# Performance work log

Hardware: AMD Instinct MI355X
Metric: run time of the kernel (lower is better)

## Reference

```python
import jax, jax.numpy as jnp
import numpy as np

N_NODES = 100000
NUM_LAYER = 3
REG_WEIGHT = 1e-4


def setup_inputs() -> dict:
    key = jax.random.key(0)
    ks = jax.random.split(key, 6)
    E = 1280000
    B = 4096
    D = 64
    # xavier-uniform-like scale for embedding table
    emb_weight = jax.random.normal(ks[0], (N_NODES, D), dtype=jnp.float32) * 0.01
    src = jax.random.randint(ks[1], (E,), 0, N_NODES, dtype=jnp.int32)
    dst = jax.random.randint(ks[2], (E,), 0, N_NODES, dtype=jnp.int32)
    users = jax.random.randint(ks[3], (B,), 0, N_NODES, dtype=jnp.int32)
    pos = jax.random.randint(ks[4], (B,), 0, N_NODES, dtype=jnp.int32)
    neg = jax.random.randint(ks[5], (B,), 0, N_NODES, dtype=jnp.int32)
    return {"emb_weight": emb_weight, "src": src, "dst": dst,
            "users": users, "pos": pos, "neg": neg}


def _edge_norm(src, dst):
    # DGL norm(): d = sum of edge mask (ones) per dst node; adj_e = d[src]^-0.5 * d[dst]^-0.5
    ones = jnp.ones(src.shape[0], dtype=jnp.float32)
    deg = jax.ops.segment_sum(ones, dst, num_segments=N_NODES)
    dinv = jnp.where(deg > 0, deg ** -0.5, 0.0)  # inf -> 0 handling
    return dinv[src] * dinv[dst]  # [E]


def _propagate(emb_weight, src, dst, adj):
    # LightGCN propagation: h_{l+1}[v] = sum_{(u->v)} adj_e * h_l[u]
    h = emb_weight
    layers = [h]
    for _ in range(NUM_LAYER):
        m = h[src] * adj[:, None]                    # [E, D] gather + edge weight
        h = jax.ops.segment_sum(m, dst, num_segments=N_NODES)  # [N, D] scatter-sum
        layers.append(h)
    return jnp.mean(jnp.stack(layers, axis=1), axis=1)  # mean over L+1 layers


def reference(emb_weight, src, dst, users, pos, neg):
    adj = _edge_norm(src, dst)
    all_emb = _propagate(emb_weight, src, dst, adj)

    u_e, p_e, n_e = all_emb[users], all_emb[pos], all_emb[neg]
    u0, p0, n0 = emb_weight[users], emb_weight[pos], emb_weight[neg]

    B = users.shape[0]
    reg_loss = 0.5 * (jnp.sum(u0 ** 2) + jnp.sum(p0 ** 2) + jnp.sum(n0 ** 2)) / B
    reg_loss = reg_loss * REG_WEIGHT

    pos_scores = jnp.sum(u_e * p_e, axis=1)
    neg_scores = jnp.sum(u_e * n_e, axis=1)
    loss_emb = jnp.mean(jax.nn.softplus(neg_scores - pos_scores))

    loss = loss_emb + reg_loss
    return loss, loss_emb, reg_loss
```

## Files before the change

### kernel.cpp

```cpp
#include <hip/hip_runtime.h>
#include <hip/hip_fp8.h>
#include <math.h>

#define N_NODES 100000
#define DIM 64
#define NUM_LAYER 3
#define BATCH 4096
#define REG_WEIGHT 1e-4f
#define NBUCKET 391
#define STAGE_CAP 4096
#define CURPAD 16
#define H_SCALE 64.0f
#define H_INV_SCALE (1.0f / 64.0f)

typedef float floatx2 __attribute__((ext_vector_type(2)));

__device__ unsigned char g_hf8[2][(size_t)N_NODES * DIM];
__device__ float g_sums[(size_t)3 * BATCH * DIM];
__device__ int   g_row_ptr[N_NODES + 1];
__device__ float g_dinv[N_NODES];
__device__ int   g_bcur[NBUCKET * CURPAD];
__device__ unsigned int g_stage[NBUCKET * STAGE_CAP];
__device__ int   g_csr[1280000];
__device__ int   g_shead[N_NODES];
__device__ int   g_snext[3 * BATCH];
__device__ float g_part_sp[BATCH];
__device__ float g_part_rg[BATCH];

__device__ inline void fma4_fp8(unsigned int d, float w,
                                float& a0, float& a1, float& a2, float& a3) {
    floatx2 lo = __builtin_amdgcn_cvt_pk_f32_fp8((int)d, false);
    floatx2 hi = __builtin_amdgcn_cvt_pk_f32_fp8((int)d, true);
    a0 = fmaf(w, lo.x, a0); a1 = fmaf(w, lo.y, a1);
    a2 = fmaf(w, hi.x, a2); a3 = fmaf(w, hi.y, a3);
}
__device__ inline unsigned int pack4_fp8(float a0, float a1, float a2, float a3) {
    int w = __builtin_amdgcn_cvt_pk_fp8_f32(a0, a1, 0, false);
    w     = __builtin_amdgcn_cvt_pk_fp8_f32(a2, a3, w, true);
    return (unsigned int)w;
}

__global__ void prelude(const float* __restrict__ emb) {
    int i = blockIdx.x * blockDim.x + threadIdx.x;
    int stride = gridDim.x * blockDim.x;
    for (int k = i; k < NBUCKET; k += stride) g_bcur[k * CURPAD] = k * STAGE_CAP;
    for (int k = i; k < N_NODES; k += stride) g_shead[k] = -1;
    const int NW = N_NODES * DIM / 4;
    unsigned int* hw = (unsigned int*)g_hf8[0];
    for (int k = i; k < NW; k += stride) {
        const float* e = emb + (size_t)k * 4;
        hw[k] = pack4_fp8(e[0] * H_SCALE, e[1] * H_SCALE,
                          e[2] * H_SCALE, e[3] * H_SCALE);
    }
}

#define EDGES_PER_THREAD 8
__global__ void __launch_bounds__(1024) stage_buckets(const int* __restrict__ src,
                                                      const int* __restrict__ dst, int E,
                                                      const int* __restrict__ users,
                                                      const int* __restrict__ pos,
                                                      const int* __restrict__ neg) {
    __shared__ int h[NBUCKET];
    __shared__ int cur[NBUCKET];
    int tid = threadIdx.x;
    int gt = blockIdx.x * 1024 + tid;
    if (gt < 3 * BATCH) {
        int which = gt / BATCH, s = gt - which * BATCH;
        const int* idx = (which == 0) ? users : ((which == 1) ? pos : neg);
        g_snext[gt] = atomicExch(&g_shead[idx[s]], gt);
    }
    int base = blockIdx.x * (1024 * EDGES_PER_THREAD);
    for (int i = tid; i < NBUCKET; i += 1024) h[i] = 0;
    __syncthreads();
    int myd[EDGES_PER_THREAD], mys[EDGES_PER_THREAD];
    #pragma unroll
    for (int k = 0; k < EDGES_PER_THREAD; ++k) {
        int e = base + k * 1024 + tid;
        if (e < E) {
            myd[k] = dst[e]; mys[k] = src[e];
            atomicAdd(&h[myd[k] >> 8], 1);
        } else myd[k] = -1;
    }
    __syncthreads();
    for (int i = tid; i < NBUCKET; i += 1024) {
        int c = h[i];
        cur[i] = c ? atomicAdd(&g_bcur[i * CURPAD], c) : 0;
    }
    __syncthreads();
    #pragma unroll
    for (int k = 0; k < EDGES_PER_THREAD; ++k) {
        if (myd[k] >= 0) {
            int p = atomicAdd(&cur[myd[k] >> 8], 1);
            g_stage[p] = (unsigned int)((mys[k] << 8) | (myd[k] & 255));
        }
    }
}

__global__ void __launch_bounds__(512) finalize_place() {
    __shared__ int cs[512];
    __shared__ int lh[256], sc[256], cur[256];
    int b = blockIdx.x, t = threadIdx.x;
    int c = (t < NBUCKET) ? (g_bcur[t * CURPAD] - t * STAGE_CAP) : 0;
    cs[t] = c;
    __syncthreads();
    for (int off = 1; off < 512; off <<= 1) {
        int x = (t >= off) ? cs[t - off] : 0;
        __syncthreads();
        cs[t] += x;
        __syncthreads();
    }
    int mybase = (b > 0) ? cs[b - 1] : 0;
    int cnt    = cs[b] - mybase;
    if (b == 0 && t == 0) g_row_ptr[N_NODES] = cs[NBUCKET - 1];
    int sbeg = b * STAGE_CAP;
    if (t < 256) lh[t] = 0;
    __syncthreads();
    for (int k = t; k < cnt; k += 512)
        atomicAdd(&lh[g_stage[sbeg + k] & 255], 1);
    __syncthreads();
    int v = 0;
    if (t < 256) { v = lh[t]; sc[t] = v; }
    __syncthreads();
    for (int off = 1; off < 256; off <<= 1) {
        int x = (t >= off && t < 256) ? sc[t - off] : 0;
        __syncthreads();
        if (t < 256) sc[t] += x;
        __syncthreads();
    }
    if (t < 256) {
        int start = mybase + sc[t] - v;
        cur[t] = start;
        int node = (b << 8) + t;
        if (node < N_NODES) {
            g_row_ptr[node] = start;
            g_dinv[node]    = (v > 0) ? rsqrtf((float)v) : 0.0f;
        }
    }
    __syncthreads();
    for (int k = t; k < cnt; k += 512) {
        unsigned int e = g_stage[sbeg + k];
        int pos = atomicAdd(&cur[e & 255], 1);
        g_csr[pos] = (int)(e >> 8);
    }
}

__global__ void pull_layer_fp8(const unsigned char* __restrict__ h,
                               unsigned char* __restrict__ hn, int do_gather) {
    int wid  = (blockIdx.x * blockDim.x + threadIdx.x) >> 6;
    int lane = threadIdx.x & 63;
    int nA = wid * 2, nB = nA + 1;
    if (nA >= N_NODES) return;
    bool hasB = (nB < N_NODES);
    int g  = lane >> 4;
    int li = lane & 15;
    int begA = g_row_ptr[nA], endA = g_row_ptr[nA + 1];
    int begB = hasB ? g_row_ptr[nB] : 0, endB = hasB ? g_row_ptr[nB + 1] : 0;
    float dinvA = g_dinv[nA];
    float dinvB = hasB ? g_dinv[nB] : 0.0f;
    int lenA = endA - begA, lenB = endB - begB;
    int maxLen = max(lenA, lenB);
    float aA0 = 0.f, aA1 = 0.f, aA2 = 0.f, aA3 = 0.f;
    float aB0 = 0.f, aB1 = 0.f, aB2 = 0.f, aB3 = 0.f;
    for (int off = 0; off < maxLen; off += 64) {
        int kA = off + lane;
        int sA = 0; float wA = 0.0f;
        if (kA < lenA) { sA = g_csr[begA + kA]; wA = g_dinv[sA] * dinvA; }
        int sB = 0; float wB = 0.0f;
        if (kA < lenB) { sB = g_csr[begB + kA]; wB = g_dinv[sB] * dinvB; }
        int cnt = min(64, maxLen - off);
        for (int j = 0; j < cnt; j += 16) {
            int   sA1 = __shfl(sA, j + g),      sA2 = __shfl(sA, j + 4 + g);
            int   sA3 = __shfl(sA, j + 8 + g),  sA4 = __shfl(sA, j + 12 + g);
            int   sB1 = __shfl(sB, j + g),      sB2 = __shfl(sB, j + 4 + g);
            int   sB3 = __shfl(sB, j + 8 + g),  sB4 = __shfl(sB, j + 12 + g);
            float wA1 = __shfl(wA, j + g),      wA2 = __shfl(wA, j + 4 + g);
            float wA3 = __shfl(wA, j + 8 + g),  wA4 = __shfl(wA, j + 12 + g);
            float wB1 = __shfl(wB, j + g),      wB2 = __shfl(wB, j + 4 + g);
            float wB3 = __shfl(wB, j + 8 + g),  wB4 = __shfl(wB, j + 12 + g);
            unsigned int dA1 = *(const unsigned int*)(h + (size_t)sA1 * DIM + li * 4);
            unsigned int dA2 = *(const unsigned int*)(h + (size_t)sA2 * DIM + li * 4);
            unsigned int dA3 = *(const unsigned int*)(h + (size_t)sA3 * DIM + li * 4);
            unsigned int dA4 = *(const unsigned int*)(h + (size_t)sA4 * DIM + li * 4);
            unsigned int dB1 = *(const unsigned int*)(h + (size_t)sB1 * DIM + li * 4);
            unsigned int dB2 = *(const unsigned int*)(h + (size_t)sB2 * DIM + li * 4);
            unsigned int dB3 = *(const unsigned int*)(h + (size_t)sB3 * DIM + li * 4);
            unsigned int dB4 = *(const unsigned int*)(h + (size_t)sB4 * DIM + li * 4);
            fma4_fp8(dA1, wA1, aA0, aA1, aA2, aA3);
            fma4_fp8(dA2, wA2, aA0, aA1, aA2, aA3);
            fma4_fp8(dA3, wA3, aA0, aA1, aA2, aA3);
            fma4_fp8(dA4, wA4, aA0, aA1, aA2, aA3);
            fma4_fp8(dB1, wB1, aB0, aB1, aB2, aB3);
            fma4_fp8(dB2, wB2, aB0, aB1, aB2, aB3);
            fma4_fp8(dB3, wB3, aB0, aB1, aB2, aB3);
            fma4_fp8(dB4, wB4, aB0, aB1, aB2, aB3);
        }
    }
    #pragma unroll
    for (int off = 16; off < 64; off <<= 1) {
        aA0 += __shfl_xor(aA0, off); aA1 += __shfl_xor(aA1, off);
        aA2 += __shfl_xor(aA2, off); aA3 += __shfl_xor(aA3, off);
        aB0 += __shfl_xor(aB0, off); aB1 += __shfl_xor(aB1, off);
        aB2 += __shfl_xor(aB2, off); aB3 += __shfl_xor(aB3, off);
    }
    if (lane < 16) {
        *(unsigned int*)(hn + (size_t)nA * DIM + li * 4) = pack4_fp8(aA0, aA1, aA2, aA3);
        if (hasB)
            *(unsigned int*)(hn + (size_t)nB * DIM + li * 4) = pack4_fp8(aB0, aB1, aB2, aB3);
    }
    if (do_gather) {
        int sidx = g_shead[nA];
        while (sidx >= 0) {
            if (lane < 16) {
                float* sp = &g_sums[(size_t)sidx * DIM + li * 4];
                sp[0] = aA0 * H_INV_SCALE; sp[1] = aA1 * H_INV_SCALE;
                sp[2] = aA2 * H_INV_SCALE; sp[3] = aA3 * H_INV_SCALE;
            }
            sidx = g_snext[sidx];
        }
        if (hasB) {
            sidx = g_shead[nB];
            while (sidx >= 0) {
                if (lane < 16) {
                    float* sp = &g_sums[(size_t)sidx * DIM + li * 4];
                    sp[0] = aB0 * H_INV_SCALE; sp[1] = aB1 * H_INV_SCALE;
                    sp[2] = aB2 * H_INV_SCALE; sp[3] = aB3 * H_INV_SCALE;
                }
                sidx = g_snext[sidx];
            }
        }
    }
}

__global__ void pull_sampled(const unsigned char* __restrict__ h,
                             const int* __restrict__ users, const int* __restrict__ pos,
                             const int* __restrict__ neg) {
    int wid  = (blockIdx.x * blockDim.x + threadIdx.x) >> 6;
    int lane = threadIdx.x & 63;
    if (wid >= 3 * BATCH) return;
    int which = wid / BATCH;
    int i     = wid - which * BATCH;
    const int* idx = (which == 0) ? users : ((which == 1) ? pos : neg);
    int node = idx[i];
    int g  = lane >> 4;
    int li = lane & 15;
    int beg = g_row_ptr[node], end = g_row_ptr[node + 1];
    float dinv_d = g_dinv[node];
    float a0 = 0.f, a1 = 0.f, a2 = 0.f, a3 = 0.f;
    for (int base = beg; base < end; base += 64) {
        int k = base + lane;
        int s = 0; float w = 0.0f;
        if (k < end) { s = g_csr[k]; w = g_dinv[s] * dinv_d; }
        int cnt = min(64, end - base);
        for (int j = 0; j < cnt; j += 16) {
            int   sA = __shfl(s, j + g),      sB = __shfl(s, j + 4 + g);
            int   sC = __shfl(s, j + 8 + g),  sD = __shfl(s, j + 12 + g);
            float wA = __shfl(w, j + g),      wB = __shfl(w, j + 4 + g);
            float wC = __shfl(w, j + 8 + g),  wD = __shfl(w, j + 12 + g);
            unsigned int dA = *(const unsigned int*)(h + (size_t)sA * DIM + li * 4);
            unsigned int dB = *(const unsigned int*)(h + (size_t)sB * DIM + li * 4);
            unsigned int dC = *(const unsigned int*)(h + (size_t)sC * DIM + li * 4);
            unsigned int dD = *(const unsigned int*)(h + (size_t)sD * DIM + li * 4);
            fma4_fp8(dA, wA, a0, a1, a2, a3);
            fma4_fp8(dB, wB, a0, a1, a2, a3);
            fma4_fp8(dC, wC, a0, a1, a2, a3);
            fma4_fp8(dD, wD, a0, a1, a2, a3);
        }
    }
    #pragma unroll
    for (int off = 16; off < 64; off <<= 1) {
        a0 += __shfl_xor(a0, off);
        a1 += __shfl_xor(a1, off);
        a2 += __shfl_xor(a2, off);
        a3 += __shfl_xor(a3, off);
    }
    if (lane < 16) {
        unsigned int dn = *(const unsigned int*)(h + (size_t)node * DIM + li * 4);
        floatx2 lo = __builtin_amdgcn_cvt_pk_f32_fp8((int)dn, false);
        floatx2 hi = __builtin_amdgcn_cvt_pk_f32_fp8((int)dn, true);
        float* sp = &g_sums[(size_t)wid * DIM + li * 4];
        sp[0] += (a0 + lo.x) * H_INV_SCALE;
        sp[1] += (a1 + lo.y) * H_INV_SCALE;
        sp[2] += (a2 + hi.x) * H_INV_SCALE;
        sp[3] += (a3 + hi.y) * H_INV_SCALE;
    }
}

__global__ void score_reduce(const float* __restrict__ emb,
                             const int* __restrict__ users, const int* __restrict__ pos,
                             const int* __restrict__ neg) {
    int wid  = (blockIdx.x * blockDim.x + threadIdx.x) >> 6;
    int lane = threadIdx.x & 63;
    if (wid >= BATCH) return;
    float u0 = emb[(size_t)users[wid] * DIM + lane];
    float p0 = emb[(size_t)pos[wid]   * DIM + lane];
    float n0 = emb[(size_t)neg[wid]   * DIM + lane];
    float u = 0.25f * (g_sums[(size_t)wid * DIM + lane] + u0);
    float p = 0.25f * (g_sums[(size_t)(BATCH + wid) * DIM + lane] + p0);
    float n = 0.25f * (g_sums[(size_t)(2 * BATCH + wid) * DIM + lane] + n0);
    float ps = u * p;
    float ns = u * n;
    float rg = u0 * u0 + p0 * p0 + n0 * n0;
    #pragma unroll
    for (int off = 32; off > 0; off >>= 1) {
        ps += __shfl_down(ps, off);
        ns += __shfl_down(ns, off);
        rg += __shfl_down(rg, off);
    }
    if (lane == 0) {
        float x  = ns - ps;
        float sp = fmaxf(x, 0.0f) + log1pf(expf(-fabsf(x)));
        g_part_sp[wid] = sp;
        g_part_rg[wid] = rg;
    }
}

__global__ void final_reduce(float* __restrict__ out) {
    __shared__ float s_sp[256], s_rg[256];
    int t = threadIdx.x;
    float sp = 0.0f, rg = 0.0f;
    for (int i = t; i < BATCH; i += 256) { sp += g_part_sp[i]; rg += g_part_rg[i]; }
    s_sp[t] = sp; s_rg[t] = rg;
    __syncthreads();
    for (int off = 128; off > 0; off >>= 1) {
        if (t < off) { s_sp[t] += s_sp[t + off]; s_rg[t] += s_rg[t + off]; }
        __syncthreads();
    }
    if (t == 0) {
        float loss_emb = s_sp[0] / (float)BATCH;
        float reg      = 0.5f * s_rg[0] / (float)BATCH * REG_WEIGHT;
        out[0] = loss_emb + reg;
        out[1] = loss_emb;
        out[2] = reg;
    }
}

extern "C" void kernel_launch(void* const* d_in, const int* in_sizes, int n_in,
                              void* d_out, int out_size, void* d_ws, size_t ws_size,
                              hipStream_t stream) {
    const float* emb   = (const float*)d_in[0];
    const int*   src   = (const int*)d_in[1];
    const int*   dst   = (const int*)d_in[2];
    const int*   users = (const int*)d_in[3];
    const int*   pos   = (const int*)d_in[4];
    const int*   neg   = (const int*)d_in[5];
    const int E = in_sizes[1];
    float* out = (float*)d_out;

    unsigned char* hf_a;  hipGetSymbolAddress((void**)&hf_a, HIP_SYMBOL(g_hf8));
    unsigned char* hf_b = hf_a + (size_t)N_NODES * DIM;

    prelude<<<1024, 256, 0, stream>>>(emb);

    const int STAGE_BLOCKS = (E + 1024 * EDGES_PER_THREAD - 1) / (1024 * EDGES_PER_THREAD);
    stage_buckets<<<STAGE_BLOCKS, 1024, 0, stream>>>(src, dst, E, users, pos, neg);
    finalize_place<<<NBUCKET, 512, 0, stream>>>();

    const int NPAIR = (N_NODES + 1) / 2;
    const int PULL_BLOCKS = (NPAIR * 64 + 255) / 256;

    pull_layer_fp8<<<PULL_BLOCKS, 256, 0, stream>>>(hf_a, hf_b, 1);

    pull_layer_fp8<<<PULL_BLOCKS, 256, 0, stream>>>(hf_b, hf_a, 0);

    pull_sampled<<<(3 * BATCH * 64 + 255) / 256, 256, 0, stream>>>(hf_a, users, pos, neg);

    score_reduce<<<(BATCH * 64 + 255) / 256, 256, 0, stream>>>(emb, users, pos, neg);
    final_reduce<<<1, 256, 0, stream>>>(out);
}
```

Before: 191.6 us.

## Fold prelude into staging kernel and reset scratch state in later kernels

Removes the separate prelude kernel. The fp8 conversion of the embedding table moves into the tail of stage_buckets. Bucket cursors now start at zero and get the bucket base added on use. The sampled-list heads switch to a 1-based encoding with 0 as empty, so zero-initialised globals are valid on the first call, and the first pull layer resets the cursors and heads for the next call. This saves one launch and the initialisation sweeps, but it depends on the first invocation seeing zero-initialised device memory and on each call restoring that state.

```diff
diff --git a/kernel.cpp b/kernel.cpp
--- a/kernel.cpp
+++ b/kernel.cpp
@@ -40,26 +40,13 @@
     return (unsigned int)w;
 }
 
-__global__ void prelude(const float* __restrict__ emb) {
-    int i = blockIdx.x * blockDim.x + threadIdx.x;
-    int stride = gridDim.x * blockDim.x;
-    for (int k = i; k < NBUCKET; k += stride) g_bcur[k * CURPAD] = k * STAGE_CAP;
-    for (int k = i; k < N_NODES; k += stride) g_shead[k] = -1;
-    const int NW = N_NODES * DIM / 4;
-    unsigned int* hw = (unsigned int*)g_hf8[0];
-    for (int k = i; k < NW; k += stride) {
-        const float* e = emb + (size_t)k * 4;
-        hw[k] = pack4_fp8(e[0] * H_SCALE, e[1] * H_SCALE,
-                          e[2] * H_SCALE, e[3] * H_SCALE);
-    }
-}
-
 #define EDGES_PER_THREAD 8
 __global__ void __launch_bounds__(1024) stage_buckets(const int* __restrict__ src,
                                                       const int* __restrict__ dst, int E,
                                                       const int* __restrict__ users,
                                                       const int* __restrict__ pos,
-                                                      const int* __restrict__ neg) {
+                                                      const int* __restrict__ neg,
+                                                      const float* __restrict__ emb) {
     __shared__ int h[NBUCKET];
     __shared__ int cur[NBUCKET];
     int tid = threadIdx.x;
@@ -67,7 +54,7 @@
     if (gt < 3 * BATCH) {
         int which = gt / BATCH, s = gt - which * BATCH;
         const int* idx = (which == 0) ? users : ((which == 1) ? pos : neg);
-        g_snext[gt] = atomicExch(&g_shead[idx[s]], gt);
+        g_snext[gt] = atomicExch(&g_shead[idx[s]], gt + 1);
     }
     int base = blockIdx.x * (1024 * EDGES_PER_THREAD);
     for (int i = tid; i < NBUCKET; i += 1024) h[i] = 0;
@@ -84,7 +71,7 @@
     __syncthreads();
     for (int i = tid; i < NBUCKET; i += 1024) {
         int c = h[i];
-        cur[i] = c ? atomicAdd(&g_bcur[i * CURPAD], c) : 0;
+        cur[i] = c ? (atomicAdd(&g_bcur[i * CURPAD], c) + i * STAGE_CAP) : 0;
     }
     __syncthreads();
     #pragma unroll
@@ -94,13 +81,23 @@
             g_stage[p] = (unsigned int)((mys[k] << 8) | (myd[k] & 255));
         }
     }
+    {
+        const int NW = N_NODES * DIM / 4;
+        int stride = gridDim.x * 1024;
+        unsigned int* hw = (unsigned int*)g_hf8[0];
+        for (int k = blockIdx.x * 1024 + tid; k < NW; k += stride) {
+            const float* e = emb + (size_t)k * 4;
+            hw[k] = pack4_fp8(e[0] * H_SCALE, e[1] * H_SCALE,
+                              e[2] * H_SCALE, e[3] * H_SCALE);
+        }
+    }
 }
 
 __global__ void __launch_bounds__(512) finalize_place() {
     __shared__ int cs[512];
     __shared__ int lh[256], sc[256], cur[256];
     int b = blockIdx.x, t = threadIdx.x;
-    int c = (t < NBUCKET) ? (g_bcur[t * CURPAD] - t * STAGE_CAP) : 0;
+    int c = (t < NBUCKET) ? g_bcur[t * CURPAD] : 0;
     cs[t] = c;
     __syncthreads();
     for (int off = 1; off < 512; off <<= 1) {
@@ -146,7 +143,9 @@
 
 __global__ void pull_layer_fp8(const unsigned char* __restrict__ h,
                                unsigned char* __restrict__ hn, int do_gather) {
-    int wid  = (blockIdx.x * blockDim.x + threadIdx.x) >> 6;
+    int gid0 = blockIdx.x * blockDim.x + threadIdx.x;
+    if (do_gather && gid0 < NBUCKET) g_bcur[gid0 * CURPAD] = 0;
+    int wid  = gid0 >> 6;
     int lane = threadIdx.x & 63;
     int nA = wid * 2, nB = nA + 1;
     if (nA >= N_NODES) return;
@@ -209,24 +208,28 @@
     }
     if (do_gather) {
         int sidx = g_shead[nA];
-        while (sidx >= 0) {
+        while (sidx > 0) {
+            int sreal = sidx - 1;
             if (lane < 16) {
-                float* sp = &g_sums[(size_t)sidx * DIM + li * 4];
+                float* sp = &g_sums[(size_t)sreal * DIM + li * 4];
                 sp[0] = aA0 * H_INV_SCALE; sp[1] = aA1 * H_INV_SCALE;
                 sp[2] = aA2 * H_INV_SCALE; sp[3] = aA3 * H_INV_SCALE;
             }
-            sidx = g_snext[sidx];
-        }
+            sidx = g_snext[sreal];
+        }
+        if (lane == 0) g_shead[nA] = 0;
         if (hasB) {
             sidx = g_shead[nB];
-            while (sidx >= 0) {
+            while (sidx > 0) {
+                int sreal = sidx - 1;
                 if (lane < 16) {
-                    float* sp = &g_sums[(size_t)sidx * DIM + li * 4];
+                    float* sp = &g_sums[(size_t)sreal * DIM + li * 4];
                     sp[0] = aB0 * H_INV_SCALE; sp[1] = aB1 * H_INV_SCALE;
                     sp[2] = aB2 * H_INV_SCALE; sp[3] = aB3 * H_INV_SCALE;
                 }
-                sidx = g_snext[sidx];
+                sidx = g_snext[sreal];
             }
+            if (lane == 0) g_shead[nB] = 0;
         }
     }
 }
@@ -349,10 +352,8 @@
     unsigned char* hf_a;  hipGetSymbolAddress((void**)&hf_a, HIP_SYMBOL(g_hf8));
     unsigned char* hf_b = hf_a + (size_t)N_NODES * DIM;
 
-    prelude<<<1024, 256, 0, stream>>>(emb);
-
     const int STAGE_BLOCKS = (E + 1024 * EDGES_PER_THREAD - 1) / (1024 * EDGES_PER_THREAD);
-    stage_buckets<<<STAGE_BLOCKS, 1024, 0, stream>>>(src, dst, E, users, pos, neg);
+    stage_buckets<<<STAGE_BLOCKS, 1024, 0, stream>>>(src, dst, E, users, pos, neg, emb);
     finalize_place<<<NBUCKET, 512, 0, stream>>>();
 
     const int NPAIR = (N_NODES + 1) / 2;
```

After: 192.6 us. About the same (+0.5%).
